# Performance work log

Hardware: AMD Instinct MI355X
Metric: run time of the kernel (lower is better)

Reference implementation:

```python
import jax, jax.numpy as jnp
import numpy as np

D = 768
H = 12
DH = D // H
DFF = 4 * D
B, S = 2, 2048


def setup_inputs() -> dict:
    key = jax.random.key(0)
    ks = jax.random.split(key, 12)
    inp = {
        "X": jax.random.normal(ks[0], (B, S, D), dtype=jnp.float32),
        # per-head projections, stacked over heads (nn.Linear: y = x W^T + b; we store W already transposed as [d, d_h])
        "Wq": jax.random.normal(ks[1], (H, D, DH), dtype=jnp.float32) * (1.0 / np.sqrt(D)),
        "bq": jnp.zeros((H, DH), dtype=jnp.float32),
        "Wk": jax.random.normal(ks[2], (H, D, DH), dtype=jnp.float32) * (1.0 / np.sqrt(D)),
        "bk": jnp.zeros((H, DH), dtype=jnp.float32),
        "Wv": jax.random.normal(ks[3], (H, D, DH), dtype=jnp.float32) * (1.0 / np.sqrt(D)),
        "bv": jnp.zeros((H, DH), dtype=jnp.float32),
        "W0": jax.random.normal(ks[4], (D, D), dtype=jnp.float32) * (1.0 / np.sqrt(D)),
        "b0": jnp.zeros((D,), dtype=jnp.float32),
        # FFN params are torch.randn (unit std) in the original
        "W1": jax.random.normal(ks[5], (D, DFF), dtype=jnp.float32),
        "b1": jnp.zeros((DFF,), dtype=jnp.float32),
        "W2": jax.random.normal(ks[6], (DFF, D), dtype=jnp.float32),
        "b2": jnp.zeros((D,), dtype=jnp.float32),
        "g1": jnp.ones((D,), dtype=jnp.float32),
        "o1": jnp.zeros((D,), dtype=jnp.float32),
        "g2": jnp.ones((D,), dtype=jnp.float32),
        "o2": jnp.zeros((D,), dtype=jnp.float32),
    }
    return inp


def _layernorm(x, gain, offset):
    # original: (x - mean) / (std + 1e-5)  with population std (unbiased=False)
    m = jnp.mean(x, axis=-1, keepdims=True)
    sd = jnp.sqrt(jnp.mean((x - m) ** 2, axis=-1, keepdims=True))
    return gain * ((x - m) / (sd + 1e-5)) + offset


def _mha(x, Wq, bq, Wk, bk, Wv, bv, W0, b0):
    # batched over heads; equivalent to the per-head SHA loop + concat
    q = jnp.einsum("bsd,hdk->bhsk", x, Wq) + bq[None, :, None, :]
    k = jnp.einsum("bsd,hdk->bhsk", x, Wk) + bk[None, :, None, :]
    v = jnp.einsum("bsd,hdk->bhsk", x, Wv) + bv[None, :, None, :]
    scores = jnp.einsum("bhsk,bhtk->bhst", q, k) / np.sqrt(DH).astype(np.float32)
    seq = x.shape[1]
    causal = jnp.tril(jnp.ones((seq, seq), dtype=bool))
    scores = jnp.where(causal[None, None], scores, -jnp.inf)
    w = jax.nn.softmax(scores, axis=-1)
    out = jnp.einsum("bhst,bhtk->bhsk", w, v)
    out = jnp.transpose(out, (0, 2, 1, 3)).reshape(x.shape[0], seq, D)  # concat heads
    return out @ W0 + b0


def reference(X, Wq, bq, Wk, bk, Wv, bv, W0, b0, W1, b1, W2, b2, g1, o1, g2, o2):
    h = X + _mha(_layernorm(X, g1, o1), Wq, bq, Wk, bk, Wv, bv, W0, b0)
    y = _layernorm(h, g2, o2)
    y = jnp.maximum(y @ W1 + b1, 0.0) @ W2 + b2
    return h + y
```

## Files before the change

### kernel.cpp

```cpp
#include <hip/hip_runtime.h>
#include <hip/hip_bf16.h>
#include <cstdint>

#define BB 2
#define SS 2048
#define DD 768
#define HH 12
#define DHH 64
#define DFF 3072
#define MM (BB * SS)

typedef __attribute__((ext_vector_type(8))) short bf16x8;
typedef __attribute__((ext_vector_type(4))) float f32x4;
typedef __attribute__((ext_vector_type(16))) float f32x16;
typedef __attribute__((ext_vector_type(4))) unsigned short u16x4;
typedef __attribute__((ext_vector_type(8))) unsigned short u16x8;
typedef unsigned int u32;

#define DEV static __device__ __forceinline__

typedef __attribute__((address_space(1))) void AS1void;
typedef __attribute__((address_space(3))) void AS3void;

DEV void async_copy16(const void* g, void* l) {
  __builtin_amdgcn_global_load_lds((AS1void*)g, (AS3void*)l, 16, 0, 0);
}

DEV unsigned short bf16bits(float f) {
  __hip_bfloat16 h = __float2bfloat16(f);
  return *(unsigned short*)&h;
}

DEV float bits2f(unsigned short u) {
  u32 x = ((u32)u) << 16;
  union { u32 u; float f; } c; c.u = x;
  return c.f;
}

DEV u32 pack2(float a, float b) {
  return ((u32)bf16bits(b) << 16) | (u32)bf16bits(a);
}

__global__ __launch_bounds__(256) void ln_kernel(
    const float* __restrict__ x, const float* __restrict__ gain,
    const float* __restrict__ off, __hip_bfloat16* __restrict__ out)
{
  const int wave = threadIdx.x >> 6;
  const int lane = threadIdx.x & 63;
  const int row = blockIdx.x * 4 + wave;
  const float* xr = x + (size_t)row * DD;

  float4 v[3];
  float s1 = 0.f, s2 = 0.f;
#pragma unroll
  for (int j = 0; j < 3; ++j) {
    v[j] = *(const float4*)(xr + (j * 64 + lane) * 4);
    s1 += v[j].x + v[j].y + v[j].z + v[j].w;
    s2 += v[j].x * v[j].x + v[j].y * v[j].y + v[j].z * v[j].z + v[j].w * v[j].w;
  }
#pragma unroll
  for (int d = 1; d < 64; d <<= 1) {
    s1 += __shfl_xor(s1, d);
    s2 += __shfl_xor(s2, d);
  }
  const float mean = s1 * (1.0f / 768.0f);
  const float var = fmaxf(s2 * (1.0f / 768.0f) - mean * mean, 0.0f);
  const float rs = 1.0f / (sqrtf(var) + 1e-5f);

  unsigned short* orow = (unsigned short*)out + (size_t)row * DD;
#pragma unroll
  for (int j = 0; j < 3; ++j) {
    const int c = (j * 64 + lane) * 4;
    float4 g4 = *(const float4*)(gain + c);
    float4 o4 = *(const float4*)(off + c);
    u16x4 pk;
    pk[0] = bf16bits(g4.x * ((v[j].x - mean) * rs) + o4.x);
    pk[1] = bf16bits(g4.y * ((v[j].y - mean) * rs) + o4.y);
    pk[2] = bf16bits(g4.z * ((v[j].z - mean) * rs) + o4.z);
    pk[3] = bf16bits(g4.w * ((v[j].w - mean) * rs) + o4.w);
    *(u16x4*)(orow + c) = pk;
  }
}

__global__ __launch_bounds__(256) void transpose_generic(
    const float* __restrict__ in, __hip_bfloat16* __restrict__ out, int R, int C)
{
  __shared__ float tile[64][65];
  const int c0 = blockIdx.x * 64, r0 = blockIdx.y * 64;
  for (int i = threadIdx.x; i < 4096; i += 256) {
    int r = i >> 6, c = i & 63;
    tile[r][c] = in[(size_t)(r0 + r) * C + c0 + c];
  }
  __syncthreads();
  for (int i = threadIdx.x; i < 4096; i += 256) {
    int c = i >> 6, r = i & 63;
    out[(size_t)(c0 + c) * R + r0 + r] = __float2bfloat16(tile[r][c]);
  }
}

__global__ __launch_bounds__(256) void transpose_qkv(
    const float* __restrict__ Wq, const float* __restrict__ Wk,
    const float* __restrict__ Wv, __hip_bfloat16* __restrict__ out)
{
  __shared__ float tile[64][65];
  const int z = blockIdx.z;
  const int p = z / HH, h = z - p * HH;
  const float* in = (p == 0 ? Wq : (p == 1 ? Wk : Wv)) + (size_t)h * DD * DHH;
  const int r0 = blockIdx.y * 64;
  for (int i = threadIdx.x; i < 4096; i += 256) {
    int r = i >> 6, c = i & 63;
    tile[r][c] = in[(size_t)(r0 + r) * DHH + c];
  }
  __syncthreads();
  for (int i = threadIdx.x; i < 4096; i += 256) {
    int c = i >> 6, r = i & 63;
    out[(size_t)(p * DD + h * DHH + c) * DD + r0 + r] = __float2bfloat16(tile[r][c]);
  }
}

__global__ __launch_bounds__(256) void kvimg_kernel(
    const __hip_bfloat16* __restrict__ qkv, char* __restrict__ kimg,
    char* __restrict__ vimg)
{
  __shared__ unsigned short tileK[64][72];
  __shared__ unsigned short tileV[64][72];
  const int bh = blockIdx.y;
  const int b = bh / HH, h = bh - (bh / HH) * HH;
  const int t0 = blockIdx.x * 64;
  const int HD = 3 * DD;
  const unsigned short* Kp = (const unsigned short*)qkv + (size_t)(b * SS) * HD + DD + h * DHH;
  const unsigned short* Vp = (const unsigned short*)qkv + (size_t)(b * SS) * HD + 2 * DD + h * DHH;
  char* kdst = kimg + ((size_t)bh * 32 + blockIdx.x) * 8192;
  char* vdst = vimg + ((size_t)bh * 32 + blockIdx.x) * 8192;

  for (int i = threadIdx.x; i < 512; i += 256) {
    const int r = i >> 3, c8 = (i & 7) * 8;
    *(bf16x8*)&tileK[r][c8] = *(const bf16x8*)(Kp + (size_t)(t0 + r) * HD + c8);
    *(bf16x8*)&tileV[r][c8] = *(const bf16x8*)(Vp + (size_t)(t0 + r) * HD + c8);
  }
  __syncthreads();
  for (int i = threadIdx.x; i < 512; i += 256) {
    const int f = i >> 6, l = i & 63;
    const int kc = f >> 1, half = f & 1;
    const int lc = l & 31, lh = l >> 5;
    *(bf16x8*)(kdst + i * 16) = *(const bf16x8*)&tileK[half * 32 + lc][kc * 16 + lh * 8];
    union { unsigned short u[8]; bf16x8 v; } w;
#pragma unroll
    for (int e = 0; e < 8; ++e) w.u[e] = tileV[kc * 16 + lh * 8 + e][half * 32 + lc];
    *(bf16x8*)(vdst + i * 16) = w.v;
  }
}

template<bool RELU, bool OUT_BF16, bool HAS_RES>
__global__ __launch_bounds__(256) void gemm_bt(
    const __hip_bfloat16* __restrict__ A, const __hip_bfloat16* __restrict__ BT,
    const float* __restrict__ bias, const float* __restrict__ res,
    void* __restrict__ outp, int M, int N, int K)
{
  __shared__ __hip_bfloat16 Alds[2][128 * 32];
  __shared__ __hip_bfloat16 Blds[2][128 * 32];
  const int tid = threadIdx.x;
  const int wave = tid >> 6;
  const int lane = tid & 63;
  const int fr = lane & 15, fq = lane >> 4;
  const int wr = wave >> 1, wc = wave & 1;
  const int bm = blockIdx.y * 128, bn = blockIdx.x * 128;

  const int srow = tid >> 2;
  const int scol = (tid & 3) * 8;
  const __hip_bfloat16* ag0 = A + (size_t)(bm + srow) * K + scol;
  const __hip_bfloat16* ag1 = A + (size_t)(bm + 64 + srow) * K + scol;
  const __hip_bfloat16* bg0 = BT + (size_t)(bn + srow) * K + scol;
  const __hip_bfloat16* bg1 = BT + (size_t)(bn + 64 + srow) * K + scol;
  const int so = wave * 512;

  f32x4 acc[4][4] = {};

  async_copy16(ag0, &Alds[0][so]);
  async_copy16(ag1, &Alds[0][2048 + so]);
  async_copy16(bg0, &Blds[0][so]);
  async_copy16(bg1, &Blds[0][2048 + so]);
  __syncthreads();

  const int niter = K / 32;
  for (int i = 0; i < niter; ++i) {
    const int cur = i & 1;
    if (i + 1 < niter) {
      const int k1 = (i + 1) * 32;
      async_copy16(ag0 + k1, &Alds[cur ^ 1][so]);
      async_copy16(ag1 + k1, &Alds[cur ^ 1][2048 + so]);
      async_copy16(bg0 + k1, &Blds[cur ^ 1][so]);
      async_copy16(bg1 + k1, &Blds[cur ^ 1][2048 + so]);
    }
    bf16x8 af[4], bfr[4];
#pragma unroll
    for (int i4 = 0; i4 < 4; ++i4)
      af[i4] = *(const bf16x8*)(&Alds[cur][(wr * 64 + i4 * 16 + fr) * 32 + fq * 8]);
#pragma unroll
    for (int j4 = 0; j4 < 4; ++j4)
      bfr[j4] = *(const bf16x8*)(&Blds[cur][(wc * 64 + j4 * 16 + fr) * 32 + fq * 8]);
#pragma unroll
    for (int i4 = 0; i4 < 4; ++i4)
#pragma unroll
      for (int j4 = 0; j4 < 4; ++j4)
        acc[i4][j4] = __builtin_amdgcn_mfma_f32_16x16x32_bf16(af[i4], bfr[j4], acc[i4][j4], 0, 0, 0);
    __syncthreads();
  }

#pragma unroll
  for (int j = 0; j < 4; ++j) {
    const int c = bn + wc * 64 + j * 16 + fr;
    const float bv = bias[c];
#pragma unroll
    for (int i = 0; i < 4; ++i) {
#pragma unroll
      for (int r = 0; r < 4; ++r) {
        const int rr = bm + wr * 64 + i * 16 + fq * 4 + r;
        float v = acc[i][j][r] + bv;
        if (RELU) v = fmaxf(v, 0.0f);
        if (HAS_RES) v += res[(size_t)rr * N + c];
        if (OUT_BF16) ((__hip_bfloat16*)outp)[(size_t)rr * N + c] = __float2bfloat16(v);
        else          ((float*)outp)[(size_t)rr * N + c] = v;
      }
    }
  }
}

__global__ __launch_bounds__(256) void gemm_bt_sk(
    const __hip_bfloat16* __restrict__ A, const __hip_bfloat16* __restrict__ BT,
    unsigned short* __restrict__ part01, unsigned short* __restrict__ part23,
    int M, int N, int K, int K_per)
{
  __shared__ __hip_bfloat16 Alds[2][128 * 32];
  __shared__ __hip_bfloat16 Blds[2][128 * 32];
  const int tid = threadIdx.x;
  const int wave = tid >> 6;
  const int lane = tid & 63;
  const int fr = lane & 15, fq = lane >> 4;
  const int wr = wave >> 1, wc = wave & 1;
  const int bm = blockIdx.y * 128, bn = blockIdx.x * 128;
  const int z = blockIdx.z;
  unsigned short* part = (z < 2 ? part01 : part23) + (size_t)(z & 1) * M * N;
  const int kbase = z * K_per;

  const int srow = tid >> 2;
  const int scol = (tid & 3) * 8;
  const __hip_bfloat16* ag0 = A + (size_t)(bm + srow) * K + scol + kbase;
  const __hip_bfloat16* ag1 = A + (size_t)(bm + 64 + srow) * K + scol + kbase;
  const __hip_bfloat16* bg0 = BT + (size_t)(bn + srow) * K + scol + kbase;
  const __hip_bfloat16* bg1 = BT + (size_t)(bn + 64 + srow) * K + scol + kbase;
  const int so = wave * 512;

  f32x4 acc[4][4] = {};

  async_copy16(ag0, &Alds[0][so]);
  async_copy16(ag1, &Alds[0][2048 + so]);
  async_copy16(bg0, &Blds[0][so]);
  async_copy16(bg1, &Blds[0][2048 + so]);
  __syncthreads();

  const int niter = K_per / 32;
  for (int i = 0; i < niter; ++i) {
    const int cur = i & 1;
    if (i + 1 < niter) {
      const int k1 = (i + 1) * 32;
      async_copy16(ag0 + k1, &Alds[cur ^ 1][so]);
      async_copy16(ag1 + k1, &Alds[cur ^ 1][2048 + so]);
      async_copy16(bg0 + k1, &Blds[cur ^ 1][so]);
      async_copy16(bg1 + k1, &Blds[cur ^ 1][2048 + so]);
    }
    bf16x8 af[4], bfr[4];
#pragma unroll
    for (int i4 = 0; i4 < 4; ++i4)
      af[i4] = *(const bf16x8*)(&Alds[cur][(wr * 64 + i4 * 16 + fr) * 32 + fq * 8]);
#pragma unroll
    for (int j4 = 0; j4 < 4; ++j4)
      bfr[j4] = *(const bf16x8*)(&Blds[cur][(wc * 64 + j4 * 16 + fr) * 32 + fq * 8]);
#pragma unroll
    for (int i4 = 0; i4 < 4; ++i4)
#pragma unroll
      for (int j4 = 0; j4 < 4; ++j4)
        acc[i4][j4] = __builtin_amdgcn_mfma_f32_16x16x32_bf16(af[i4], bfr[j4], acc[i4][j4], 0, 0, 0);
    __syncthreads();
  }

#pragma unroll
  for (int j = 0; j < 4; ++j) {
    const int c = bn + wc * 64 + j * 16 + fr;
#pragma unroll
    for (int i = 0; i < 4; ++i) {
#pragma unroll
      for (int r = 0; r < 4; ++r) {
        const int rr = bm + wr * 64 + i * 16 + fq * 4 + r;
        part[(size_t)rr * N + c] = bf16bits(acc[i][j][r]);
      }
    }
  }
}

__global__ __launch_bounds__(256) void combine4(
    const unsigned short* __restrict__ part01, const unsigned short* __restrict__ part23,
    const float* __restrict__ res, const float* __restrict__ bias,
    float* __restrict__ out, int MN, int N)
{
  const int idx = (blockIdx.x * 256 + threadIdx.x) * 4;
  if (idx >= MN) return;
  const u16x4 a0 = *(const u16x4*)(part01 + idx);
  const u16x4 a1 = *(const u16x4*)(part01 + MN + idx);
  const u16x4 a2 = *(const u16x4*)(part23 + idx);
  const u16x4 a3 = *(const u16x4*)(part23 + MN + idx);
  const float4 rr = *(const float4*)(res + idx);
  const float4 bb = *(const float4*)(bias + (idx % N));
  float4 o;
  o.x = bits2f(a0[0]) + bits2f(a1[0]) + bits2f(a2[0]) + bits2f(a3[0]) + rr.x + bb.x;
  o.y = bits2f(a0[1]) + bits2f(a1[1]) + bits2f(a2[1]) + bits2f(a3[1]) + rr.y + bb.y;
  o.z = bits2f(a0[2]) + bits2f(a1[2]) + bits2f(a2[2]) + bits2f(a3[2]) + rr.z + bb.z;
  o.w = bits2f(a0[3]) + bits2f(a1[3]) + bits2f(a2[3]) + bits2f(a3[3]) + rr.w + bb.w;
  *(float4*)(out + idx) = o;
}

__global__ __launch_bounds__(128, 3) void attn_kernel(
    const __hip_bfloat16* __restrict__ qkv, const char* __restrict__ kimg,
    const char* __restrict__ vimg, __hip_bfloat16* __restrict__ outp)
{
  const int HD = 3 * DD;
  const int id = blockIdx.x;
  const int xcd = id & 7;
  const int j = id >> 3;
  const int s2 = 63 - j / 3;
  const int bhl = j - 3 * (j / 3);
  const int bh = xcd * 3 + bhl;
  const int b = bh / HH, h = bh - (bh / HH) * HH;

  const int q0w = s2 * 32;
  const int tid = threadIdx.x;
  const int c = tid >> 6;
  const int lane = tid & 63;
  const int col = lane & 31, hi = lane >> 5;
  const int qg = q0w + col;

  const size_t base = (size_t)b * SS * HD;
  const __hip_bfloat16* Qp = qkv + base + h * DHH;
  const char* kimg_h = kimg + (size_t)bh * 32 * 8192;
  const char* vimg_h = vimg + (size_t)bh * 32 * 8192;

  __shared__ __align__(16) char sm[17408];

  bf16x8 qf[4];
#pragma unroll
  for (int kc = 0; kc < 4; ++kc)
    qf[kc] = *(const bf16x8*)(Qp + (size_t)qg * HD + kc * 16 + hi * 8);

  f32x16 o0 = {}, o1 = {};
  float mreg = -1e30f, lreg = 0.f;
  const float CS = 0.125f * 1.44269504f;

  const int ntiles = (q0w >> 6) + 1;

  bf16x8 kf[8];
  {
    const char* ks = kimg_h + (size_t)c * 8192 + lane * 16;
#pragma unroll
    for (int f = 0; f < 8; ++f) kf[f] = *(const bf16x8*)(ks + f * 1024);
  }

  for (int t = c; t < ntiles; t += 2) {
    const int kv0 = t * 64;
    f32x16 s0 = {}, s1 = {};
    __builtin_amdgcn_s_setprio(1);
#pragma unroll
    for (int kc = 0; kc < 4; ++kc) {
      s0 = __builtin_amdgcn_mfma_f32_32x32x16_bf16(kf[kc * 2],     qf[kc], s0, 0, 0, 0);
      s1 = __builtin_amdgcn_mfma_f32_32x32x16_bf16(kf[kc * 2 + 1], qf[kc], s1, 0, 0, 0);
    }
    __builtin_amdgcn_s_setprio(0);
    bf16x8 vf[8];
    {
      const char* vs = vimg_h + (size_t)t * 8192 + lane * 16;
#pragma unroll
      for (int f = 0; f < 8; ++f) vf[f] = *(const bf16x8*)(vs + f * 1024);
    }
    if (t + 2 < ntiles) {
      const char* ks = kimg_h + (size_t)(t + 2) * 8192 + lane * 16;
#pragma unroll
      for (int f = 0; f < 8; ++f) kf[f] = *(const bf16x8*)(ks + f * 1024);
    }
    if (kv0 + 63 > q0w) {
#pragma unroll
      for (int r = 0; r < 16; ++r) {
        const int tl = (r & 3) + 8 * (r >> 2) + 4 * hi;
        s0[r] = (kv0 + tl <= qg) ? s0[r] : -1e30f;
        s1[r] = (kv0 + 32 + tl <= qg) ? s1[r] : -1e30f;
      }
    }
    float mx = s0[0];
#pragma unroll
    for (int r = 1; r < 16; ++r) mx = fmaxf(mx, s0[r]);
#pragma unroll
    for (int r = 0; r < 16; ++r) mx = fmaxf(mx, s1[r]);
    mx = fmaxf(mx, __shfl_xor(mx, 32));
    const float mnew = fmaxf(mreg, mx);
    const float alpha = exp2f((mreg - mnew) * CS);
    mreg = mnew;
    const float mc = mnew * CS;
    float ps = 0.f;
#pragma unroll
    for (int r = 0; r < 16; ++r) {
      const float p0 = exp2f(s0[r] * CS - mc); s0[r] = p0; ps += p0;
      const float p1 = exp2f(s1[r] * CS - mc); s1[r] = p1; ps += p1;
    }
    ps += __shfl_xor(ps, 32);
    lreg = lreg * alpha + ps;
#pragma unroll
    for (int r = 0; r < 16; ++r) { o0[r] *= alpha; o1[r] *= alpha; }

    u32 pk0[4][2], pk1[4][2];
#pragma unroll
    for (int qd = 0; qd < 4; ++qd) {
      pk0[qd][0] = pack2(s0[4 * qd + 0], s0[4 * qd + 1]);
      pk0[qd][1] = pack2(s0[4 * qd + 2], s0[4 * qd + 3]);
      pk1[qd][0] = pack2(s1[4 * qd + 0], s1[4 * qd + 1]);
      pk1[qd][1] = pack2(s1[4 * qd + 2], s1[4 * qd + 3]);
    }
#pragma unroll
    for (int kc = 0; kc < 4; ++kc) {
      const int qa = 2 * (kc & 1), qb = qa + 1;
      const u32 A0 = (kc < 2) ? pk0[qa][0] : pk1[qa][0];
      const u32 A1 = (kc < 2) ? pk0[qa][1] : pk1[qa][1];
      const u32 B0 = (kc < 2) ? pk0[qb][0] : pk1[qb][0];
      const u32 B1 = (kc < 2) ? pk0[qb][1] : pk1[qb][1];
      const u32 send0 = hi ? A0 : B0;
      const u32 send1 = hi ? A1 : B1;
      const u32 recv0 = __shfl_xor(send0, 32);
      const u32 recv1 = __shfl_xor(send1, 32);
      const u32 su0 = hi ? B0 : A0;
      const u32 su1 = hi ? B1 : A1;
      union { u32 u[4]; bf16x8 v; } pf;
      pf.u[0] = hi ? recv0 : su0;
      pf.u[1] = hi ? recv1 : su1;
      pf.u[2] = hi ? su0 : recv0;
      pf.u[3] = hi ? su1 : recv1;
      __builtin_amdgcn_s_setprio(1);
      o0 = __builtin_amdgcn_mfma_f32_32x32x16_bf16(vf[kc * 2],     pf.v, o0, 0, 0, 0);
      o1 = __builtin_amdgcn_mfma_f32_32x32x16_bf16(vf[kc * 2 + 1], pf.v, o1, 0, 0, 0);
      __builtin_amdgcn_s_setprio(0);
    }
  }

  float* opart = (float*)sm;
  float* mlp   = (float*)(sm + 16640);
#pragma unroll
  for (int r = 0; r < 16; ++r) {
    const int d = (r & 3) + 8 * (r >> 2) + 4 * hi;
    opart[(c * 32 + col) * 65 + d]      = o0[r];
    opart[(c * 32 + col) * 65 + d + 32] = o1[r];
  }
  if (hi == 0) {
    mlp[c * 64 + col]      = mreg;
    mlp[c * 64 + 32 + col] = lreg;
  }
  __syncthreads();

  const int q = tid >> 2;
  const int d0 = (tid & 3) * 16;
  float mcv[2], lcv[2];
#pragma unroll
  for (int cc = 0; cc < 2; ++cc) {
    mcv[cc] = mlp[cc * 64 + q];
    lcv[cc] = mlp[cc * 64 + 32 + q];
  }
  const float mstar = fmaxf(mcv[0], mcv[1]);
  float av[2], lstar = 0.f;
#pragma unroll
  for (int cc = 0; cc < 2; ++cc) {
    av[cc] = exp2f((mcv[cc] - mstar) * CS);
    lstar += av[cc] * lcv[cc];
  }
  const float inv = 1.0f / lstar;
  float acc[16] = {};
#pragma unroll
  for (int cc = 0; cc < 2; ++cc) {
    const float a = av[cc];
#pragma unroll
    for (int e = 0; e < 16; ++e)
      acc[e] += a * opart[(cc * 32 + q) * 65 + d0 + e];
  }
  unsigned short* orow = (unsigned short*)outp +
      (size_t)(b * SS + q0w + q) * DD + h * DHH + d0;
  u16x8 w8;
#pragma unroll
  for (int e = 0; e < 8; ++e) w8[e] = bf16bits(acc[e] * inv);
  *(u16x8*)orow = w8;
#pragma unroll
  for (int e = 0; e < 8; ++e) w8[e] = bf16bits(acc[8 + e] * inv);
  *(u16x8*)(orow + 8) = w8;
}

extern "C" void kernel_launch(void* const* d_in, const int* in_sizes, int n_in,
                              void* d_out, int out_size, void* d_ws, size_t ws_size,
                              hipStream_t stream)
{
  (void)in_sizes; (void)n_in; (void)out_size; (void)ws_size;
  const float* X  = (const float*)d_in[0];
  const float* Wq = (const float*)d_in[1];
  const float* bq = (const float*)d_in[2];
  const float* Wk = (const float*)d_in[3];
  const float* bk = (const float*)d_in[4];
  const float* Wv = (const float*)d_in[5];
  const float* bv = (const float*)d_in[6];
  const float* W0 = (const float*)d_in[7];
  const float* b0 = (const float*)d_in[8];
  const float* W1 = (const float*)d_in[9];
  const float* b1 = (const float*)d_in[10];
  const float* W2 = (const float*)d_in[11];
  const float* b2 = (const float*)d_in[12];
  const float* g1 = (const float*)d_in[13];
  const float* o1 = (const float*)d_in[14];
  const float* g2 = (const float*)d_in[15];
  const float* o2 = (const float*)d_in[16];

  char* ws = (char*)d_ws;
  auto alloc = [&](size_t bytes) {
    char* p = ws;
    ws += (bytes + 255) & ~(size_t)255;
    return p;
  };
  __hip_bfloat16* ln1    = (__hip_bfloat16*)alloc((size_t)MM * DD * 2);
  __hip_bfloat16* qkvb16 = (__hip_bfloat16*)alloc((size_t)MM * 3 * DD * 2);
  __hip_bfloat16* attnb  = (__hip_bfloat16*)alloc((size_t)MM * DD * 2);
  float*          hbuf   = (float*)alloc((size_t)MM * DD * 4);
  __hip_bfloat16* ln2    = (__hip_bfloat16*)alloc((size_t)MM * DD * 2);
  __hip_bfloat16* ffn1   = (__hip_bfloat16*)alloc((size_t)MM * DFF * 2);
  __hip_bfloat16* WqkvT  = (__hip_bfloat16*)alloc((size_t)3 * DD * DD * 2);
  __hip_bfloat16* W0T    = (__hip_bfloat16*)alloc((size_t)DD * DD * 2);
  __hip_bfloat16* W1T    = (__hip_bfloat16*)alloc((size_t)DFF * DD * 2);
  __hip_bfloat16* W2T    = (__hip_bfloat16*)alloc((size_t)DD * DFF * 2);
  float*          qkvbias= (float*)alloc((size_t)3 * DD * 4);
  unsigned short* part23 = (unsigned short*)alloc((size_t)2 * MM * DD * 2);
  char*           kimg   = alloc((size_t)24 * 32 * 8192);
  char*           vimg   = alloc((size_t)24 * 32 * 8192);
  unsigned short* part01 = (unsigned short*)ln1;

  transpose_qkv<<<dim3(1, 12, 36), 256, 0, stream>>>(Wq, Wk, Wv, WqkvT);
  transpose_generic<<<dim3(12, 12), 256, 0, stream>>>(W0, W0T, DD, DD);
  transpose_generic<<<dim3(48, 12), 256, 0, stream>>>(W1, W1T, DD, DFF);
  transpose_generic<<<dim3(12, 48), 256, 0, stream>>>(W2, W2T, DFF, DD);
  hipMemcpyAsync(qkvbias,          bq, DD * 4, hipMemcpyDeviceToDevice, stream);
  hipMemcpyAsync(qkvbias + DD,     bk, DD * 4, hipMemcpyDeviceToDevice, stream);
  hipMemcpyAsync(qkvbias + 2 * DD, bv, DD * 4, hipMemcpyDeviceToDevice, stream);

  ln_kernel<<<MM / 4, 256, 0, stream>>>(X, g1, o1, ln1);
  gemm_bt<false, true, false><<<dim3(3 * DD / 128, MM / 128), 256, 0, stream>>>(
      ln1, WqkvT, qkvbias, nullptr, qkvb16, MM, 3 * DD, DD);
  kvimg_kernel<<<dim3(SS / 64, BB * HH), 256, 0, stream>>>(qkvb16, kimg, vimg);
  attn_kernel<<<1536, 128, 0, stream>>>(qkvb16, kimg, vimg, attnb);
  gemm_bt<false, false, true><<<dim3(DD / 128, MM / 128), 256, 0, stream>>>(
      attnb, W0T, b0, X, hbuf, MM, DD, DD);
  ln_kernel<<<MM / 4, 256, 0, stream>>>(hbuf, g2, o2, ln2);
  gemm_bt<true, true, false><<<dim3(DFF / 128, MM / 128), 256, 0, stream>>>(
      ln2, W1T, b1, nullptr, ffn1, MM, DFF, DD);
  gemm_bt_sk<<<dim3(DD / 128, MM / 128, 4), 256, 0, stream>>>(
      ffn1, W2T, part01, part23, MM, DD, DFF, DFF / 4);
  combine4<<<(MM * DD) / 1024, 256, 0, stream>>>(
      part01, part23, hbuf, b2, (float*)d_out, MM * DD, DD);
}
```

Before: 201.2 us.

## Split-K the output projection and fuse combine with residual and LayerNorm

```diff
diff --git a/kernel.cpp b/kernel.cpp
--- a/kernel.cpp
+++ b/kernel.cpp
@@ -317,6 +317,61 @@
   o.z = bits2f(a0[2]) + bits2f(a1[2]) + bits2f(a2[2]) + bits2f(a3[2]) + rr.z + bb.z;
   o.w = bits2f(a0[3]) + bits2f(a1[3]) + bits2f(a2[3]) + bits2f(a3[3]) + rr.w + bb.w;
   *(float4*)(out + idx) = o;
+}
+
+__global__ __launch_bounds__(256) void combine2_ln(
+    const unsigned short* __restrict__ part, const float* __restrict__ res,
+    const float* __restrict__ bias, const float* __restrict__ gain,
+    const float* __restrict__ off, float* __restrict__ hout,
+    __hip_bfloat16* __restrict__ lnout)
+{
+  const int wave = threadIdx.x >> 6;
+  const int lane = threadIdx.x & 63;
+  const int row = blockIdx.x * 4 + wave;
+  const int MN = MM * DD;
+  const size_t rbase = (size_t)row * DD;
+
+  float v[3][4];
+  float s1 = 0.f, s2 = 0.f;
+#pragma unroll
+  for (int j = 0; j < 3; ++j) {
+    const int c = (j * 64 + lane) * 4;
+    const size_t idx = rbase + c;
+    const u16x4 a0 = *(const u16x4*)(part + idx);
+    const u16x4 a1 = *(const u16x4*)(part + MN + idx);
+    const float4 rr = *(const float4*)(res + idx);
+    const float4 bb = *(const float4*)(bias + c);
+    v[j][0] = bits2f(a0[0]) + bits2f(a1[0]) + rr.x + bb.x;
+    v[j][1] = bits2f(a0[1]) + bits2f(a1[1]) + rr.y + bb.y;
+    v[j][2] = bits2f(a0[2]) + bits2f(a1[2]) + rr.z + bb.z;
+    v[j][3] = bits2f(a0[3]) + bits2f(a1[3]) + rr.w + bb.w;
+    float4 hv = { v[j][0], v[j][1], v[j][2], v[j][3] };
+    *(float4*)(hout + idx) = hv;
+    s1 += v[j][0] + v[j][1] + v[j][2] + v[j][3];
+    s2 += v[j][0]*v[j][0] + v[j][1]*v[j][1] + v[j][2]*v[j][2] + v[j][3]*v[j][3];
+  }
+#pragma unroll
+  for (int d = 1; d < 64; d <<= 1) {
+    s1 += __shfl_xor(s1, d);
+    s2 += __shfl_xor(s2, d);
+  }
+  const float mean = s1 * (1.0f / 768.0f);
+  const float var = fmaxf(s2 * (1.0f / 768.0f) - mean * mean, 0.0f);
+  const float rs = 1.0f / (sqrtf(var) + 1e-5f);
+
+  unsigned short* orow = (unsigned short*)lnout + rbase;
+#pragma unroll
+  for (int j = 0; j < 3; ++j) {
+    const int c = (j * 64 + lane) * 4;
+    const float4 g4 = *(const float4*)(gain + c);
+    const float4 o4 = *(const float4*)(off + c);
+    u16x4 pk;
+    pk[0] = bf16bits(g4.x * ((v[j][0] - mean) * rs) + o4.x);
+    pk[1] = bf16bits(g4.y * ((v[j][1] - mean) * rs) + o4.y);
+    pk[2] = bf16bits(g4.z * ((v[j][2] - mean) * rs) + o4.z);
+    pk[3] = bf16bits(g4.w * ((v[j][3] - mean) * rs) + o4.w);
+    *(u16x4*)(orow + c) = pk;
+  }
 }
 
 __global__ __launch_bounds__(128, 3) void attn_kernel(
@@ -554,9 +609,10 @@
       ln1, WqkvT, qkvbias, nullptr, qkvb16, MM, 3 * DD, DD);
   kvimg_kernel<<<dim3(SS / 64, BB * HH), 256, 0, stream>>>(qkvb16, kimg, vimg);
   attn_kernel<<<1536, 128, 0, stream>>>(qkvb16, kimg, vimg, attnb);
-  gemm_bt<false, false, true><<<dim3(DD / 128, MM / 128), 256, 0, stream>>>(
-      attnb, W0T, b0, X, hbuf, MM, DD, DD);
-  ln_kernel<<<MM / 4, 256, 0, stream>>>(hbuf, g2, o2, ln2);
+  gemm_bt_sk<<<dim3(DD / 128, MM / 128, 2), 256, 0, stream>>>(
+      attnb, W0T, part23, part23, MM, DD, DD, DD / 2);
+  combine2_ln<<<MM / 4, 256, 0, stream>>>(
+      part23, X, b0, g2, o2, hbuf, ln2);
   gemm_bt<true, true, false><<<dim3(DFF / 128, MM / 128), 256, 0, stream>>>(
       ln2, W1T, b1, nullptr, ffn1, MM, DFF, DD);
   gemm_bt_sk<<<dim3(DD / 128, MM / 128, 4), 256, 0, stream>>>(
```

New measurement: 198.1 us, median of 2. No clear change (-1.5%).
